# Optimization experiments

Hardware: AMD Instinct MI355X
Metric: run time of the kernel (lower is better)

## Reference

```python
import jax, jax.numpy as jnp
import numpy as np

NUM_HEADS = 16
THETA = 10000.0


def _rope(x, cos, sin):
    # x: [B, H, S, d_k]; cos/sin: [S, d_k//2] broadcast over B, H
    x1 = x[..., 0::2]
    x2 = x[..., 1::2]
    r1 = cos * x1 - sin * x2
    r2 = sin * x1 + cos * x2
    # interleave back: (..., half_d, 2) -> (..., d_k)
    return jnp.stack((r1, r2), axis=-1).reshape(x.shape)


def setup_inputs() -> dict:
    key = jax.random.key(0)
    ks = jax.random.split(key, 5)
    B, S, D = 4, 2048, 1024
    scale = D ** -0.5
    x = jax.random.normal(ks[0], (B, S, D), dtype=jnp.float32)
    wq = jax.random.normal(ks[1], (D, D), dtype=jnp.float32) * scale
    wk = jax.random.normal(ks[2], (D, D), dtype=jnp.float32) * scale
    wv = jax.random.normal(ks[3], (D, D), dtype=jnp.float32) * scale
    wo = jax.random.normal(ks[4], (D, D), dtype=jnp.float32) * scale
    return {"x": x, "wq": wq, "wk": wk, "wv": wv, "wo": wo}


def reference(x, wq, wk, wv, wo):
    B, S, D = x.shape
    H = NUM_HEADS
    dk = D // H

    def proj(w):
        # x @ w.T, split heads -> [B, H, S, dk]
        y = jnp.einsum('bsd,ed->bse', x, w)
        return y.reshape(B, S, H, dk).transpose(0, 2, 1, 3)

    q, k, v = proj(wq), proj(wk), proj(wv)

    # RoPE (interleaved pairs), positions = arange(S)
    inv_freq = THETA ** (-(jnp.arange(0, dk, 2, dtype=jnp.float32) / dk))
    ang = jnp.arange(S, dtype=jnp.float32)[:, None] * inv_freq  # [S, dk//2]
    cos, sin = jnp.cos(ang), jnp.sin(ang)
    q = _rope(q, cos, sin)
    k = _rope(k, cos, sin)

    scores = jnp.einsum('bhqd,bhkd->bhqk', q, k) / jnp.sqrt(jnp.asarray(dk, x.dtype))
    causal = jnp.tril(jnp.ones((S, S), dtype=bool))  # keep self + past
    scores = jnp.where(causal, scores, -jnp.inf)
    p = jax.nn.softmax(scores, axis=-1)
    attn = jnp.einsum('bhqk,bhkd->bhqd', p, v)
    attn = attn.transpose(0, 2, 1, 3).reshape(B, S, D)
    return jnp.einsum('bsd,ed->bse', attn, wo)
```

## Files before the change

kernel.cpp:

```cpp
#include <hip/hip_runtime.h>
#include <hip/hip_bf16.h>
#include <cstdint>
#include <cstddef>

#define Bb 4
#define Ss 2048
#define Dd 1024
#define Hh 16
#define Mm (Bb*Ss)

typedef __bf16 bf16_t;
typedef __bf16 bf16x8 __attribute__((ext_vector_type(8)));
typedef __bf16 bf16x4 __attribute__((ext_vector_type(4)));
typedef float  f32x4  __attribute__((ext_vector_type(4)));
typedef float  f32x16 __attribute__((ext_vector_type(16)));
typedef unsigned int u32x4 __attribute__((ext_vector_type(4)));
typedef unsigned int u32x2 __attribute__((ext_vector_type(2)));

#define MFMA16(a,b,c) __builtin_amdgcn_mfma_f32_16x16x32_bf16(a,b,c,0,0,0)
#define MFMA32(a,b,c) __builtin_amdgcn_mfma_f32_32x32x16_bf16(a,b,c,0,0,0)

#define QSCALE 0.18033688011112042f

static __device__ __forceinline__ float fexp2(float x) {
#if __has_builtin(__builtin_amdgcn_exp2f)
  return __builtin_amdgcn_exp2f(x);
#else
  return exp2f(x);
#endif
}

static __device__ __forceinline__ bf16x8 ld16g(const bf16_t* p) {
  return __builtin_bit_cast(bf16x8, *reinterpret_cast<const u32x4*>(p));
}

static __device__ __forceinline__ void gload_lds16(const bf16_t* g, bf16_t* l) {
  __builtin_amdgcn_global_load_lds(
      (__attribute__((address_space(1))) void*)(g),
      (__attribute__((address_space(3))) void*)(l),
      16, 0, 0);
}

__global__ void cvt_f32_bf16(const float* __restrict__ in, bf16_t* __restrict__ out) {
  int i = (blockIdx.x * blockDim.x + threadIdx.x) * 4;
  float4 f = *reinterpret_cast<const float4*>(in + i);
  out[i + 0] = (bf16_t)f.x;
  out[i + 1] = (bf16_t)f.y;
  out[i + 2] = (bf16_t)f.z;
  out[i + 3] = (bf16_t)f.w;
}

__global__ void cvt_w4(const float* __restrict__ w0, const float* __restrict__ w1,
                       const float* __restrict__ w2, const float* __restrict__ w3,
                       bf16_t* __restrict__ out) {
  int bid = blockIdx.x;
  int seg = bid >> 10, local = bid & 1023;
  const float* w = (seg == 0) ? w0 : (seg == 1) ? w1 : (seg == 2) ? w2 : w3;
  int i = (local * 256 + threadIdx.x) * 4;
  float4 f = *reinterpret_cast<const float4*>(w + i);
  bf16_t* o = out + (size_t)seg * (Dd * Dd) + i;
  o[0] = (bf16_t)f.x; o[1] = (bf16_t)f.y; o[2] = (bf16_t)f.z; o[3] = (bf16_t)f.w;
}

__global__ void rope_tab_k(float2* __restrict__ tab) {
  int idx = blockIdx.x * 256 + threadIdx.x;
  int i = idx & 31, s = idx >> 5;
  float inv_freq = exp2f(-(float)i * (13.2877123795494f / 32.0f));
  float ang = (float)s * inv_freq;
  float sn, cs;
  sincosf(ang, &sn, &cs);
  tab[idx] = make_float2(cs, sn);
}

template <typename OutT>
__global__ __launch_bounds__(256) void gemm_bt(const bf16_t* __restrict__ A,
                                               const bf16_t* __restrict__ Bm,
                                               OutT* __restrict__ C0,
                                               OutT* __restrict__ C1,
                                               OutT* __restrict__ C2,
                                               const float2* __restrict__ tab,
                                               int Kdim) {
  __shared__ bf16_t As[2][128 * 32];
  __shared__ bf16_t Bs[2][128 * 32];
  const int t = threadIdx.x;
  const int lane = t & 63, w = t >> 6;
  const int l15 = lane & 15, lg = lane >> 4;
  const int m0 = blockIdx.x * 128, n0 = blockIdx.y * 128;
  const int wr = w >> 1, wc = w & 1;

  f32x4 acc[4][4] = {};

  auto stage = [&](int buf, int kt) {
    const int k0 = kt * 32;
#pragma unroll
    for (int c = 0; c < 2; ++c) {
      int flat = (c * 256 + t) * 16;
      int row = flat >> 6;
      int ke = (flat & 63) >> 1;
      const bf16_t* ga = A  + (size_t)(m0 + row) * Kdim + k0 + ke;
      const bf16_t* gb = Bm + (size_t)(n0 + row) * Kdim + k0 + ke;
      bf16_t* la = &As[buf][c * 2048 + w * 512];
      bf16_t* lb = &Bs[buf][c * 2048 + w * 512];
      gload_lds16(ga, la);
      gload_lds16(gb, lb);
    }
  };

  const int KT = Kdim / 32;
  stage(0, 0);
  __syncthreads();
  int buf = 0;
  for (int kt = 0; kt < KT; ++kt) {
    if (kt + 1 < KT) stage(buf ^ 1, kt + 1);
    bf16x8 af[4], bfr[4];
#pragma unroll
    for (int i = 0; i < 4; ++i) {
      af[i]  = __builtin_bit_cast(bf16x8, *reinterpret_cast<const u32x4*>(
                  &As[buf][(wr * 64 + i * 16 + l15) * 32 + lg * 8]));
      bfr[i] = __builtin_bit_cast(bf16x8, *reinterpret_cast<const u32x4*>(
                  &Bs[buf][(wc * 64 + i * 16 + l15) * 32 + lg * 8]));
    }
#pragma unroll
    for (int i = 0; i < 4; ++i)
#pragma unroll
      for (int j = 0; j < 4; ++j)
        acc[i][j] = MFMA16(af[i], bfr[j], acc[i][j]);
    __syncthreads();
    buf ^= 1;
  }

  OutT* Cs = (n0 < 1024) ? C0 : (n0 < 2048 ? C1 : C2);
  const int nb = n0 & 1023;
  const bool doRope = (tab != nullptr) && (n0 < 2048);
  const float qs = (n0 < 1024) ? QSCALE : 1.0f;

  if (doRope) {
#pragma unroll
    for (int i = 0; i < 4; ++i) {
      int rowb = m0 + wr * 64 + i * 16 + lg * 4;
#pragma unroll
      for (int j = 0; j < 4; ++j) {
        int col = nb + wc * 64 + j * 16 + l15;
        int i0 = (col & 63) >> 1;
        const bool ev = !(col & 1);
#pragma unroll
        for (int r = 0; r < 4; ++r) {
          float v = acc[i][j][r];
          float px = __shfl_xor(v, 1);
          int s = (rowb + r) & (Ss - 1);
          float2 f = tab[s * 32 + i0];
          float sn = ev ? -f.y : f.y;
          Cs[(size_t)(rowb + r) * 1024 + col] = (OutT)((f.x * v + sn * px) * qs);
        }
      }
    }
  } else {
#pragma unroll
    for (int i = 0; i < 4; ++i) {
      int rowb = m0 + wr * 64 + i * 16 + lg * 4;
#pragma unroll
      for (int j = 0; j < 4; ++j) {
        int col = nb + wc * 64 + j * 16 + l15;
#pragma unroll
        for (int r = 0; r < 4; ++r)
          Cs[(size_t)(rowb + r) * 1024 + col] = (OutT)acc[i][j][r];
      }
    }
  }
}

__global__ __launch_bounds__(256) void transpose_v(const bf16_t* __restrict__ V,
                                                   bf16_t* __restrict__ Vt) {
  __shared__ bf16_t tile[64][72];
  int bh = blockIdx.y;
  int b = bh >> 4, h = bh & 15;
  int s0 = blockIdx.x * 64;
  int t = threadIdx.x;
  const bf16_t* vbase = V + (size_t)b * Ss * Dd + h * 64;
#pragma unroll
  for (int c = 0; c < 2; ++c) {
    int cf = c * 256 + t;
    int s = cf >> 3, d8 = cf & 7;
    u32x4 v = *reinterpret_cast<const u32x4*>(vbase + (size_t)(s0 + s) * Dd + d8 * 8);
    *reinterpret_cast<u32x4*>(&tile[s][d8 * 8]) = v;
  }
  __syncthreads();
  bf16_t* obase = Vt + (size_t)bh * 64 * Ss;
#pragma unroll
  for (int c = 0; c < 2; ++c) {
    int cf = c * 256 + t;
    int d = cf >> 3, s8 = cf & 7;
    __align__(16) bf16_t tmp[8];
#pragma unroll
    for (int i = 0; i < 8; ++i) tmp[i] = tile[s8 * 8 + i][d];
    *reinterpret_cast<u32x4*>(obase + (size_t)d * Ss + s0 + s8 * 8) =
        *reinterpret_cast<const u32x4*>(tmp);
  }
}

__global__ __launch_bounds__(256, 2) void attn_k(const bf16_t* __restrict__ Q,
                                                 const bf16_t* __restrict__ K,
                                                 const bf16_t* __restrict__ Vt,
                                                 bf16_t* __restrict__ O) {
  __shared__ bf16_t Ks[3][4096];
  __shared__ bf16_t Vs[3][4096];
  const int t = threadIdx.x, lane = t & 63, w = t >> 6;
  const int l31 = lane & 31, hi = lane >> 5, hi8 = hi * 8;
  const int bh = blockIdx.y, b = bh >> 4, h = bh & 15;
  const int bx = blockIdx.x;
  const int i = bx * 4 + w;
  const int q0a = 32 * i, q0b = 2016 - 32 * i;
  const int dtA = q0a >> 6, hfA = (q0a >> 5) & 1;
  const int dtB = q0b >> 6, hfB = (q0b >> 5) & 1;
  const int NT = 32 - 2 * bx;
  const bf16_t* qb = Q + (size_t)b * Ss * Dd + h * 64;
  const bf16_t* kb = K + (size_t)b * Ss * Dd + h * 64;
  const bf16_t* vtb = Vt + (size_t)bh * 64 * Ss;

  const int a_ = l31 >> 2, c_ = l31 & 3;
  const int tau = (a_ >> 1) + 2 * (a_ & 1) + ((a_ & 4) >> 1);
  const int sig = c_ + 4 * tau;

  int kfoff[4];
#pragma unroll
  for (int c = 0; c < 4; ++c) {
    int j = sig >> 1, u = (sig & 1) * 8 + c * 2 + hi;
    kfoff[c] = j * 128 + ((u ^ j) * 8);
  }
  int vfoff[2][2];
#pragma unroll
  for (int db = 0; db < 2; ++db)
#pragma unroll
    for (int ks = 0; ks < 2; ++ks) {
      int d = db * 32 + l31, j = d >> 2, u = (d & 3) * 4 + ks * 2 + hi;
      vfoff[db][ks] = j * 128 + ((u ^ j) * 8);
    }

  const int sj = t >> 4, ss = t & 15, su = ss ^ sj;
  const bf16_t* ksrc0 = kb + (size_t)(2 * sj + (su >> 3)) * Dd + (su & 7) * 8;
  const bf16_t* vsrc0 = vtb + (size_t)(4 * sj + (su >> 2)) * Ss + (su & 3) * 8;

  auto stage = [&](int buf, int kb0) {
    bf16_t* kd = &Ks[buf][w * 512];
    bf16_t* vd = &Vs[buf][w * 512];
    gload_lds16(ksrc0 + (size_t)kb0 * Dd, kd);
    gload_lds16(ksrc0 + (size_t)(kb0 + 32) * Dd, kd + 2048);
    gload_lds16(vsrc0 + kb0, vd);
    gload_lds16(vsrc0 + kb0 + 32, vd + 2048);
  };

  bf16x8 qf[2][4];
#pragma unroll
  for (int c = 0; c < 4; ++c) {
    qf[0][c] = ld16g(qb + (size_t)(q0a + l31) * Dd + c * 16 + hi8);
    qf[1][c] = ld16g(qb + (size_t)(q0b + l31) * Dd + c * 16 + hi8);
  }

  float l_[2] = {0.f, 0.f};
  f32x16 o_[2][2] = {};

  auto chain = [&](int kt, int dt, int hf, bf16x8 (&qc)[4],
                   f32x16& o0, f32x16& o1, float& lc,
                   bf16x8 (&kf)[2][4], bf16x8 (&vf)[2][2][2]) {
    if (kt > dt) return;
    const bool last = (kt == dt);
    const bool do1 = !(last && hf == 0);
    f32x16 s0 = {}, s1 = {};
    __builtin_amdgcn_s_setprio(1);
    s0 = MFMA32(kf[0][0], qc[0], s0);
    s0 = MFMA32(kf[0][1], qc[1], s0);
    s0 = MFMA32(kf[0][2], qc[2], s0);
    s0 = MFMA32(kf[0][3], qc[3], s0);
    if (do1) {
      s1 = MFMA32(kf[1][0], qc[0], s1);
      s1 = MFMA32(kf[1][1], qc[1], s1);
      s1 = MFMA32(kf[1][2], qc[2], s1);
      s1 = MFMA32(kf[1][3], qc[3], s1);
    }
    __builtin_amdgcn_s_setprio(0);
    if (last) {
      if (hf) {
#pragma unroll
        for (int reg = 0; reg < 16; ++reg) {
          const int koff = (reg & 3) + 4 * (reg >> 2) + 8 * ((reg >> 2) >> 1) + hi8;
          s1[reg] = (koff <= l31) ? s1[reg] : -INFINITY;
        }
      } else {
#pragma unroll
        for (int reg = 0; reg < 16; ++reg) {
          const int koff = (reg & 3) + 4 * (reg >> 2) + 8 * ((reg >> 2) >> 1) + hi8;
          s0[reg] = (koff <= l31) ? s0[reg] : -INFINITY;
        }
      }
    }
    float p0[16], p1[16];
#pragma unroll
    for (int r = 0; r < 16; ++r) p0[r] = fexp2(s0[r]);
    bf16x8 pa0, pa1, pb0, pb1;
#pragma unroll
    for (int r = 0; r < 8; ++r) { pa0[r] = (bf16_t)p0[r]; pa1[r] = (bf16_t)p0[r + 8]; }
    if (do1) {
#pragma unroll
      for (int r = 0; r < 16; ++r) p1[r] = fexp2(s1[r]);
#pragma unroll
      for (int r = 0; r < 8; ++r) { pb0[r] = (bf16_t)p1[r]; pb1[r] = (bf16_t)p1[r + 8]; }
#pragma unroll
      for (int r = 0; r < 16; ++r) p0[r] += p1[r];
    }
#pragma unroll
    for (int st2 = 8; st2 > 0; st2 >>= 1)
#pragma unroll
      for (int r = 0; r < st2; ++r) p0[r] += p0[r + st2];
    lc += p0[0];
    __builtin_amdgcn_s_setprio(1);
    o0 = MFMA32(vf[0][0][0], pa0, o0);
    o0 = MFMA32(vf[0][0][1], pa1, o0);
    o1 = MFMA32(vf[0][1][0], pa0, o1);
    o1 = MFMA32(vf[0][1][1], pa1, o1);
    if (do1) {
      o0 = MFMA32(vf[1][0][0], pb0, o0);
      o0 = MFMA32(vf[1][0][1], pb1, o0);
      o1 = MFMA32(vf[1][1][0], pb0, o1);
      o1 = MFMA32(vf[1][1][1], pb1, o1);
    }
    __builtin_amdgcn_s_setprio(0);
  };

  stage(0, 0);
  stage(1, 64);
  for (int j = 0; j < NT; ++j) {
    if (j == NT - 1) {
      asm volatile("s_waitcnt vmcnt(0) lgkmcnt(0)" ::: "memory");
    } else {
      asm volatile("s_waitcnt vmcnt(4) lgkmcnt(0)" ::: "memory");
    }
    __builtin_amdgcn_s_barrier();
    if (j + 2 < NT) stage((j + 2) % 3, (j + 2) * 64);
    const bf16_t* kbuf = &Ks[j % 3][0];
    const bf16_t* vbuf = &Vs[j % 3][0];
    bf16x8 kf[2][4], vf[2][2][2];
#pragma unroll
    for (int st = 0; st < 2; ++st)
#pragma unroll
      for (int c = 0; c < 4; ++c)
        kf[st][c] = __builtin_bit_cast(bf16x8,
            *reinterpret_cast<const u32x4*>(kbuf + st * 2048 + kfoff[c]));
#pragma unroll
    for (int st = 0; st < 2; ++st)
#pragma unroll
      for (int db = 0; db < 2; ++db)
#pragma unroll
        for (int ks = 0; ks < 2; ++ks)
          vf[st][db][ks] = __builtin_bit_cast(bf16x8,
              *reinterpret_cast<const u32x4*>(vbuf + st * 2048 + vfoff[db][ks]));
    chain(j, dtA, hfA, qf[0], o_[0][0], o_[0][1], l_[0], kf, vf);
    chain(j, dtB, hfB, qf[1], o_[1][0], o_[1][1], l_[1], kf, vf);
  }

#pragma unroll
  for (int ch = 0; ch < 2; ++ch) {
    const float ltot = l_[ch] + __shfl_xor(l_[ch], 32);
    const float inv = 1.0f / ltot;
    const size_t rowoff = ((size_t)b * Ss + (ch ? q0b : q0a) + l31) * Dd + h * 64;
#pragma unroll
    for (int db = 0; db < 2; ++db)
#pragma unroll
      for (int tt = 0; tt < 4; ++tt) {
        bf16x4 ov;
#pragma unroll
        for (int c = 0; c < 4; ++c) ov[c] = (bf16_t)(o_[ch][db][4 * tt + c] * inv);
        *reinterpret_cast<u32x2*>(&O[rowoff + db * 32 + 8 * tt + 4 * hi]) =
            __builtin_bit_cast(u32x2, ov);
      }
  }
}

extern "C" void kernel_launch(void* const* d_in, const int* in_sizes, int n_in,
                              void* d_out, int out_size, void* d_ws, size_t ws_size,
                              hipStream_t stream) {
  (void)in_sizes; (void)n_in; (void)out_size; (void)ws_size;
  const float* x  = (const float*)d_in[0];
  const float* wq = (const float*)d_in[1];
  const float* wk = (const float*)d_in[2];
  const float* wv = (const float*)d_in[3];
  const float* wo = (const float*)d_in[4];
  float* out = (float*)d_out;

  char* ws = (char*)d_ws;
  const size_t MB16 = 16u << 20;
  bf16_t* xb   = (bf16_t*)(ws + 0);
  bf16_t* Qb   = (bf16_t*)(ws + 1 * MB16);
  bf16_t* Kb   = (bf16_t*)(ws + 2 * MB16);
  bf16_t* Vb   = (bf16_t*)(ws + 3 * MB16);
  bf16_t* wqkv = (bf16_t*)(ws + 4 * MB16);
  bf16_t* wob  = wqkv + 3u * Dd * Dd;
  float2* tab  = (float2*)(ws + 4 * MB16 + (8u << 20));
  bf16_t* Vt   = xb;
  bf16_t* AOb  = Vb;

  cvt_f32_bf16<<<(Mm * Dd) / 1024, 256, 0, stream>>>(x, xb);
  cvt_w4<<<4096, 256, 0, stream>>>(wq, wk, wv, wo, wqkv);
  rope_tab_k<<<256, 256, 0, stream>>>(tab);

  gemm_bt<bf16_t><<<dim3(Mm / 128, 24), 256, 0, stream>>>(xb, wqkv, Qb, Kb, Vb,
                                                          tab, Dd);

  transpose_v<<<dim3(Ss / 64, Bb * Hh), 256, 0, stream>>>(Vb, Vt);

  attn_k<<<dim3(8, Bb * Hh), 256, 0, stream>>>(Qb, Kb, Vt, AOb);

  gemm_bt<float><<<dim3(Mm / 128, 8), 256, 0, stream>>>(AOb, wob, out, out, out,
                                                        nullptr, Dd);
}
```

Measured before the change: 177.9 us.

## Rewrite projection GEMM with 256x128 tiles, triple-buffered LDS and swizzled layout

Replaces the 128x128 double-buffered GEMM with a 512-thread kernel computing 256x128 tiles. It uses a three-slot LDS ring with explicit vmcnt waits, so loads for step j+2 are in flight while step j computes, and only one barrier runs per k-step. An XOR swizzle on LDS chunks is meant to cut bank conflicts on fragment reads, and s_setprio raises wave priority around the MFMA block. The larger tile halves the block count, which may reduce occupancy and tail balance for the smaller output projection (256 blocks).

```diff
diff --git a/kernel.cpp b/kernel.cpp
--- a/kernel.cpp
+++ b/kernel.cpp
@@ -73,60 +73,79 @@
 }
 
 template <typename OutT>
-__global__ __launch_bounds__(256) void gemm_bt(const bf16_t* __restrict__ A,
-                                               const bf16_t* __restrict__ Bm,
-                                               OutT* __restrict__ C0,
-                                               OutT* __restrict__ C1,
-                                               OutT* __restrict__ C2,
-                                               const float2* __restrict__ tab,
-                                               int Kdim) {
-  __shared__ bf16_t As[2][128 * 32];
-  __shared__ bf16_t Bs[2][128 * 32];
+__global__ __launch_bounds__(512, 2) void gemm2(const bf16_t* __restrict__ A,
+                                                const bf16_t* __restrict__ Bm,
+                                                OutT* __restrict__ C0,
+                                                OutT* __restrict__ C1,
+                                                OutT* __restrict__ C2,
+                                                const float2* __restrict__ tab,
+                                                int Kdim) {
+  __shared__ bf16_t As[3][256 * 32];
+  __shared__ bf16_t Bs[3][128 * 32];
   const int t = threadIdx.x;
   const int lane = t & 63, w = t >> 6;
   const int l15 = lane & 15, lg = lane >> 4;
-  const int m0 = blockIdx.x * 128, n0 = blockIdx.y * 128;
   const int wr = w >> 1, wc = w & 1;
+  const int m0 = blockIdx.x * 256, n0 = blockIdx.y * 128;
+
+  const int qa0 = t, qa1 = 512 + t;
+  const int ra0 = qa0 >> 2, sa0 = (qa0 & 3) ^ ((ra0 >> 1) & 3);
+  const int ra1 = qa1 >> 2, sa1 = (qa1 & 3) ^ ((ra1 >> 1) & 3);
+  const int rb0 = t >> 2,   sb0 = (t & 3) ^ ((rb0 >> 1) & 3);
+  const bf16_t* gA0 = A  + (size_t)(m0 + ra0) * Kdim + sa0 * 8;
+  const bf16_t* gA1 = A  + (size_t)(m0 + ra1) * Kdim + sa1 * 8;
+  const bf16_t* gB0 = Bm + (size_t)(n0 + rb0) * Kdim + sb0 * 8;
+  const int wb = (w * 64) * 8;
+
+  auto stage = [&](int slot, int kb0) {
+    gload_lds16(gA0 + kb0, &As[slot][wb]);
+    gload_lds16(gA1 + kb0, &As[slot][4096 + wb]);
+    gload_lds16(gB0 + kb0, &Bs[slot][wb]);
+  };
+
+  int aoff[4], boff[4];
+#pragma unroll
+  for (int i = 0; i < 4; ++i) {
+    int row = wr * 64 + i * 16 + l15;
+    aoff[i] = row * 32 + ((lg ^ ((row >> 1) & 3)) * 8);
+  }
+#pragma unroll
+  for (int j = 0; j < 4; ++j) {
+    int row = wc * 64 + j * 16 + l15;
+    boff[j] = row * 32 + ((lg ^ ((row >> 1) & 3)) * 8);
+  }
 
   f32x4 acc[4][4] = {};
-
-  auto stage = [&](int buf, int kt) {
-    const int k0 = kt * 32;
-#pragma unroll
-    for (int c = 0; c < 2; ++c) {
-      int flat = (c * 256 + t) * 16;
-      int row = flat >> 6;
-      int ke = (flat & 63) >> 1;
-      const bf16_t* ga = A  + (size_t)(m0 + row) * Kdim + k0 + ke;
-      const bf16_t* gb = Bm + (size_t)(n0 + row) * Kdim + k0 + ke;
-      bf16_t* la = &As[buf][c * 2048 + w * 512];
-      bf16_t* lb = &Bs[buf][c * 2048 + w * 512];
-      gload_lds16(ga, la);
-      gload_lds16(gb, lb);
-    }
-  };
-
   const int KT = Kdim / 32;
+
   stage(0, 0);
-  __syncthreads();
-  int buf = 0;
-  for (int kt = 0; kt < KT; ++kt) {
-    if (kt + 1 < KT) stage(buf ^ 1, kt + 1);
-    bf16x8 af[4], bfr[4];
-#pragma unroll
-    for (int i = 0; i < 4; ++i) {
-      af[i]  = __builtin_bit_cast(bf16x8, *reinterpret_cast<const u32x4*>(
-                  &As[buf][(wr * 64 + i * 16 + l15) * 32 + lg * 8]));
-      bfr[i] = __builtin_bit_cast(bf16x8, *reinterpret_cast<const u32x4*>(
-                  &Bs[buf][(wc * 64 + i * 16 + l15) * 32 + lg * 8]));
-    }
+  stage(1, 32);
+  for (int j = 0; j < KT; ++j) {
+    if (j == KT - 1) {
+      asm volatile("s_waitcnt vmcnt(0) lgkmcnt(0)" ::: "memory");
+    } else {
+      asm volatile("s_waitcnt vmcnt(3) lgkmcnt(0)" ::: "memory");
+    }
+    __builtin_amdgcn_s_barrier();
+    if (j + 2 < KT) stage((j + 2) % 3, (j + 2) * 32);
+    const bf16_t* ab = As[j % 3];
+    const bf16_t* bb = Bs[j % 3];
+    bf16x8 a[4], b[4];
 #pragma unroll
     for (int i = 0; i < 4; ++i)
-#pragma unroll
-      for (int j = 0; j < 4; ++j)
-        acc[i][j] = MFMA16(af[i], bfr[j], acc[i][j]);
-    __syncthreads();
-    buf ^= 1;
+      a[i] = __builtin_bit_cast(bf16x8,
+               *reinterpret_cast<const u32x4*>(ab + aoff[i]));
+#pragma unroll
+    for (int jj = 0; jj < 4; ++jj)
+      b[jj] = __builtin_bit_cast(bf16x8,
+               *reinterpret_cast<const u32x4*>(bb + boff[jj]));
+    __builtin_amdgcn_s_setprio(1);
+#pragma unroll
+    for (int i = 0; i < 4; ++i)
+#pragma unroll
+      for (int jj = 0; jj < 4; ++jj)
+        acc[i][jj] = MFMA16(a[i], b[jj], acc[i][jj]);
+    __builtin_amdgcn_s_setprio(0);
   }
 
   OutT* Cs = (n0 < 1024) ? C0 : (n0 < 2048 ? C1 : C2);
@@ -402,13 +421,13 @@
   cvt_w4<<<4096, 256, 0, stream>>>(wq, wk, wv, wo, wqkv);
   rope_tab_k<<<256, 256, 0, stream>>>(tab);
 
-  gemm_bt<bf16_t><<<dim3(Mm / 128, 24), 256, 0, stream>>>(xb, wqkv, Qb, Kb, Vb,
-                                                          tab, Dd);
+  gemm2<bf16_t><<<dim3(Mm / 256, 24), 512, 0, stream>>>(xb, wqkv, Qb, Kb, Vb,
+                                                        tab, Dd);
 
   transpose_v<<<dim3(Ss / 64, Bb * Hh), 256, 0, stream>>>(Vb, Vt);
 
   attn_k<<<dim3(8, Bb * Hh), 256, 0, stream>>>(Qb, Kb, Vt, AOb);
 
-  gemm_bt<float><<<dim3(Mm / 128, 8), 256, 0, stream>>>(AOb, wob, out, out, out,
-                                                        nullptr, Dd);
-}
+  gemm2<float><<<dim3(Mm / 256, 8), 512, 0, stream>>>(AOb, wob, out, out, out,
+                                                      nullptr, Dd);
+}
```

New measurement: 185.9 us. 4.5% more time.
